# Kernel tuning notes

Measured on AMD Instinct MI355X. Metric: run time of the kernel, lower is better.

## Reference

```python
import jax, jax.numpy as jnp
import numpy as np

B, C2D, C3D, H, W, N = 4, 64, 64, 256, 256, 16384
NEG_SLOPE = 0.1


def _conv1x1_lrelu(x, w, b):
    # 1x1 conv (no norm) + leaky_relu(0.1), per Conv2dNormRelu defaults
    y = jnp.einsum('bchw,oc->bohw', x, w) + b[None, :, None, None]
    return jax.nn.leaky_relu(y, NEG_SLOPE)


def _batch_gather(feat, idx):
    # feat: [B, C, N], idx: [B, P] -> [B, C, P]
    return jnp.take_along_axis(feat, idx[:, None, :], axis=2)


def setup_inputs() -> dict:
    key = jax.random.key(0)
    ks = jax.random.split(key, 14)
    f = jax.random.normal
    s = 0.05
    return {
        'xy': jax.random.uniform(ks[0], (B, 2, N), jnp.float32) * jnp.float32(W),
        'feat_2d': f(ks[1], (B, C2D, H, W), jnp.float32),
        'feat_3d': f(ks[2], (B, C3D, N), jnp.float32),
        'last_flow_2d': f(ks[3], (B, 2, H, W), jnp.float32),
        'last_flow_3d_to_2d': f(ks[4], (B, 2, N), jnp.float32),
        'nn_proj': jax.random.randint(ks[5], (B, H, W, 1), 0, N, jnp.int32),
        'w1': f(ks[6], (C3D, C3D + 5), jnp.float32) * s,
        'b1': f(ks[7], (C3D,), jnp.float32) * s,
        'w2': f(ks[8], (C3D, C3D), jnp.float32) * s,
        'b2': f(ks[9], (C3D,), jnp.float32) * s,
        'w3': f(ks[10], (C3D, C3D), jnp.float32) * s,
        'b3': f(ks[11], (C3D,), jnp.float32) * s,
        'wf': f(ks[12], (C2D, C2D + C3D), jnp.float32) * s,
        'bf': f(ks[13], (C2D,), jnp.float32) * s,
    }


def reference(xy, feat_2d, feat_3d, last_flow_2d, last_flow_3d_to_2d, nn_proj,
              w1, b1, w2, b2, w3, b3, wf, bf):
    b, _, h, w = feat_2d.shape
    # concat per-point flow onto 3D features: [B, C3D+2, N]
    feat_3d_aug = jnp.concatenate([feat_3d, last_flow_3d_to_2d], axis=1)

    idx = nn_proj[..., 0].reshape(b, h * w)  # nearest-neighbor point per pixel
    gathered = _batch_gather(feat_3d_aug, idx).reshape(b, -1, h, w)  # [B, C3D+2, H, W]
    xy_proj = _batch_gather(xy, idx).reshape(b, 2, h, w)             # [B, 2, H, W]

    # pixel-coordinate mesh grid: channel 0 = x (width), channel 1 = y (height)
    gy, gx = jnp.meshgrid(jnp.arange(h, dtype=xy.dtype), jnp.arange(w, dtype=xy.dtype), indexing='ij')
    grid = jnp.stack([gx, gy], axis=0)[None]  # [1, 2, H, W]
    offset = xy_proj - grid                    # [B, 2, H, W]

    # correlation between gathered 3D feats and 2D feats (channel mean)
    corr = jnp.mean(gathered[:, :C2D] * feat_2d, axis=1, keepdims=True)  # [B, 1, H, W]

    # last 2 channels are the projected flow; subtract detached last_flow_2d
    flow_ch = gathered[:, -2:] - jax.lax.stop_gradient(last_flow_2d)
    x = jnp.concatenate([corr, offset, gathered[:, :-2], flow_ch], axis=1)  # [B, C3D+5, H, W]

    x = _conv1x1_lrelu(x, w1, b1)
    x = _conv1x1_lrelu(x, w2, b2)
    x = _conv1x1_lrelu(x, w3, b3)
    out = _conv1x1_lrelu(jnp.concatenate([x, feat_2d], axis=1), wf, bf)  # [B, C2D, H, W]
    return out
```

## Files before the change

### kernel.cpp

```cpp
#include <hip/hip_runtime.h>

#define BB 4
#define CH 64
#define HW 65536
#define NN 16384
#define NT 128
#define XPITCH 104
#define LPITCH 72
#define W1OFS 0
#define W2OFS 6144
#define W3OFS 10240
#define WFOFS 14336
#define FWS_BYTE 46080
#define PTAB_BYTE 49152
#define PT_ROW 160
#define WS_NEED ((size_t)PTAB_BYTE + (size_t)BB * NN * PT_ROW)

typedef __attribute__((ext_vector_type(8))) short short8;
typedef __attribute__((ext_vector_type(4))) float f32x4;

union frag_u { unsigned short u[8]; short8 v; };
union row_u  { uint4 q[4]; unsigned short u[32]; };
union half_u { uint4 q[2]; unsigned short u[16]; };

static __device__ __forceinline__ unsigned short f2bf(float x) {
    unsigned int u = __float_as_uint(x);
    return (unsigned short)((u + 0x7fffu + ((u >> 16) & 1u)) >> 16);
}
static __device__ __forceinline__ float bf2f(unsigned short h) {
    return __uint_as_float(((unsigned int)h) << 16);
}

__global__ __launch_bounds__(256) void prep_w(
    const float* __restrict__ w1, const float* __restrict__ b1,
    const float* __restrict__ w2, const float* __restrict__ b2,
    const float* __restrict__ w3, const float* __restrict__ b3,
    const float* __restrict__ wf, const float* __restrict__ bf,
    unsigned short* __restrict__ wpk, float* __restrict__ fws)
{
    const int t = threadIdx.x;
    const int blk = blockIdx.x;
    if (blk == 0) {
        for (int i = t; i < 64 * 96; i += 256) {
            const int m = i / 96, k = i % 96;
            float v = 0.f;
            if (k < 64) v = w1[m * 69 + 3 + k];
            else if (k == 64) v = w1[m * 69 + 0];
            else if (k == 67) v = w1[m * 69 + 67];
            else if (k == 68) v = w1[m * 69 + 68];
            wpk[W1OFS + i] = f2bf(v);
        }
    } else if (blk == 1) {
        for (int i = t; i < 64 * 64; i += 256) wpk[W2OFS + i] = f2bf(w2[i]);
    } else if (blk == 2) {
        for (int i = t; i < 64 * 64; i += 256) wpk[W3OFS + i] = f2bf(w3[i]);
    } else if (blk == 3) {
        for (int i = t; i < 64 * 128; i += 256) wpk[WFOFS + i] = f2bf(wf[i]);
    } else if (t < 64) {
        fws[t]       = b1[t];
        fws[64 + t]  = b2[t];
        fws[128 + t] = b3[t];
        fws[192 + t] = bf[t];
        fws[256 + t] = w1[t * 69 + 1];
        fws[320 + t] = w1[t * 69 + 2];
    }
}

__global__ __launch_bounds__(256) void prep_t(
    const float* __restrict__ xy, const float* __restrict__ f3d,
    const float* __restrict__ lf3d, char* __restrict__ pt)
{
    const int t = threadIdx.x;
    const int cq = t >> 6;
    const int l = t & 63;
    const int gn = blockIdx.x * 64 + l;
    const int b = blockIdx.y;
    half_u r;
#pragma unroll
    for (int i = 0; i < 16; i++)
        r.u[i] = f2bf(f3d[(size_t)(b * CH + cq * 16 + i) * NN + gn]);
    char* row = pt + ((size_t)b * NN + gn) * PT_ROW;
    uint4* rq = (uint4*)row;
    rq[2 * cq] = r.q[0];
    rq[2 * cq + 1] = r.q[1];
    if (cq == 0) {
        float4 e;
        e.x = xy[(size_t)(b * 2 + 0) * NN + gn];
        e.y = xy[(size_t)(b * 2 + 1) * NN + gn];
        e.z = lf3d[(size_t)(b * 2 + 0) * NN + gn];
        e.w = lf3d[(size_t)(b * 2 + 1) * NN + gn];
        *(float4*)(row + 144) = e;
    }
}

template<int KT, int KROW, bool LO>
static __device__ __forceinline__ void layer_mfma(
    const unsigned short* __restrict__ wrow,
    const unsigned short* Xh, const unsigned short* Xl,
    int w, int ln, int q, f32x4 acc[4][2])
{
#pragma unroll
    for (int kt = 0; kt < KT; kt++) {
        const int kcol = kt * 32 + q * 8;
        short8 A[4];
#pragma unroll
        for (int mi = 0; mi < 4; mi++)
            A[mi] = *(const short8*)(wrow + (mi * 16 + ln) * KROW + kcol);
#pragma unroll
        for (int ni = 0; ni < 2; ni++) {
            const int nr = 32 * w + ni * 16 + ln;
            short8 bh = *(const short8*)(Xh + nr * XPITCH + kcol);
            short8 bl = bh;
            if (LO) bl = *(const short8*)(Xl + nr * LPITCH + kcol);
#pragma unroll
            for (int mi = 0; mi < 4; mi++) {
                acc[mi][ni] = __builtin_amdgcn_mfma_f32_16x16x32_bf16(A[mi], bh, acc[mi][ni], 0, 0, 0);
                if (LO)
                    acc[mi][ni] = __builtin_amdgcn_mfma_f32_16x16x32_bf16(A[mi], bl, acc[mi][ni], 0, 0, 0);
            }
        }
    }
}

static __device__ __forceinline__ void zero_acc(f32x4 acc[4][2]) {
#pragma unroll
    for (int mi = 0; mi < 4; mi++)
#pragma unroll
        for (int ni = 0; ni < 2; ni++)
#pragma unroll
            for (int r = 0; r < 4; r++) acc[mi][ni][r] = 0.f;
}

static __device__ __forceinline__ void epi_x(
    f32x4 acc[4][2], const float* __restrict__ fws, int bofs, bool off_fix,
    const float* offsp, unsigned short* Xh, unsigned short* Xl,
    int w, int ln, int q)
{
#pragma unroll
    for (int mi = 0; mi < 4; mi++) {
        const float4 bias = *(const float4*)(fws + bofs + mi * 16 + q * 4);
        float4 wox = bias, woy = bias;
        if (off_fix) {
            wox = *(const float4*)(fws + 256 + mi * 16 + q * 4);
            woy = *(const float4*)(fws + 320 + mi * 16 + q * 4);
        }
#pragma unroll
        for (int ni = 0; ni < 2; ni++) {
            const int nr = 32 * w + ni * 16 + ln;
            float ox = 0.f, oy = 0.f;
            if (off_fix) { ox = offsp[nr]; oy = offsp[NT + nr]; }
            unsigned int hh0 = 0, hh1 = 0, ll0 = 0, ll1 = 0;
#pragma unroll
            for (int r = 0; r < 4; r++) {
                float a = acc[mi][ni][r] + ((const float*)&bias)[r];
                if (off_fix) a += ((const float*)&wox)[r] * ox + ((const float*)&woy)[r] * oy;
                a = fmaxf(a, 0.1f * a);
                const unsigned short hb = f2bf(a);
                const unsigned short lb = f2bf(a - bf2f(hb));
                if (r == 0) { hh0 = hb; ll0 = lb; }
                if (r == 1) { hh0 |= ((unsigned)hb) << 16; ll0 |= ((unsigned)lb) << 16; }
                if (r == 2) { hh1 = hb; ll1 = lb; }
                if (r == 3) { hh1 |= ((unsigned)hb) << 16; ll1 |= ((unsigned)lb) << 16; }
            }
            *(uint2*)&Xh[nr * XPITCH + mi * 16 + q * 4] = make_uint2(hh0, hh1);
            *(uint2*)&Xl[nr * LPITCH + mi * 16 + q * 4] = make_uint2(ll0, ll1);
        }
    }
}

__global__ __launch_bounds__(256, 3) void fuse(
    const float* __restrict__ feat2d, const float* __restrict__ lf2d,
    const int* __restrict__ nn,
    const unsigned short* __restrict__ wpk, const float* __restrict__ fws,
    const char* __restrict__ ptab,
    float* __restrict__ out)
{
    __shared__ unsigned short Xhi[NT * XPITCH];
    __shared__ unsigned short Xlo[NT * LPITCH];
    __shared__ float offsS[2 * NT];

    const int tid = threadIdx.x;
    const int w = tid >> 6, lane = tid & 63;
    const int q = lane >> 4, ln = lane & 15;
    const int b = blockIdx.y;
    const int p0 = blockIdx.x * NT;

    {
        const int cp = lane >> 5, j = lane & 31;
        const int n = 32 * w + j;
        const int p = p0 + n;
        const int idx = nn[(size_t)b * HW + p];
        const char* prow = ptab + ((size_t)b * NN + idx) * PT_ROW;
        row_u g;
#pragma unroll
        for (int k = 0; k < 4; k++) g.q[k] = ((const uint4*)prow)[cp * 4 + k];
        float ca = 0.f;
#pragma unroll
        for (int i = 0; i < 32; i++) {
            const int c = cp * 32 + i;
            ca += feat2d[(size_t)(b * CH + c) * HW + p] * bf2f(g.u[i]);
        }
        uint4* xp = (uint4*)&Xhi[n * XPITCH + cp * 32];
#pragma unroll
        for (int k = 0; k < 4; k++) xp[k] = g.q[k];
        ca += __shfl_xor(ca, 32);
        if (cp == 0) {
            const float4 e = *(const float4*)(prow + 144);
            offsS[n] = e.x - (float)(p & 255);
            offsS[NT + n] = e.y - (float)(p >> 8);
            const float fcx = e.z - lf2d[(size_t)(b * 2 + 0) * HW + p];
            const float fcy = e.w - lf2d[(size_t)(b * 2 + 1) * HW + p];
            const unsigned short chh = f2bf(ca * (1.0f / 64.0f));
            const unsigned short xhh = f2bf(fcx);
            const unsigned short yhh = f2bf(fcy);
            uint4* tp = (uint4*)&Xhi[n * XPITCH + 64];
            tp[0] = make_uint4((unsigned)chh, ((unsigned)xhh) << 16, (unsigned)yhh, 0u);
            tp[1] = make_uint4(0, 0, 0, 0);
            tp[2] = make_uint4(0, 0, 0, 0);
            tp[3] = make_uint4(0, 0, 0, 0);
        }
    }

    f32x4 acc[4][2];
    zero_acc(acc);
    layer_mfma<3, 96, false>(wpk + W1OFS, Xhi, Xlo, w, ln, q, acc);
    epi_x(acc, fws, 0, true, offsS, Xhi, Xlo, w, ln, q);
    zero_acc(acc);
    layer_mfma<2, 64, true>(wpk + W2OFS, Xhi, Xlo, w, ln, q, acc);
    epi_x(acc, fws, 64, false, offsS, Xhi, Xlo, w, ln, q);
    zero_acc(acc);
    layer_mfma<2, 64, true>(wpk + W3OFS, Xhi, Xlo, w, ln, q, acc);
    epi_x(acc, fws, 128, false, offsS, Xhi, Xlo, w, ln, q);
    zero_acc(acc);
    layer_mfma<2, 128, true>(wpk + WFOFS, Xhi, Xlo, w, ln, q, acc);
#pragma unroll
    for (int kt = 2; kt < 4; kt++) {
        const int kcol = kt * 32 + q * 8;
        short8 A[4];
#pragma unroll
        for (int mi = 0; mi < 4; mi++)
            A[mi] = *(const short8*)(wpk + WFOFS + (mi * 16 + ln) * 128 + kcol);
#pragma unroll
        for (int ni = 0; ni < 2; ni++) {
            frag_u fh;
#pragma unroll
            for (int j = 0; j < 8; j++) {
                const int c = (kt - 2) * 32 + q * 8 + j;
                const float v = feat2d[(size_t)(b * CH + c) * HW + p0 + 32 * w + ni * 16 + ln];
                fh.u[j] = f2bf(v);
            }
#pragma unroll
            for (int mi = 0; mi < 4; mi++)
                acc[mi][ni] = __builtin_amdgcn_mfma_f32_16x16x32_bf16(A[mi], fh.v, acc[mi][ni], 0, 0, 0);
        }
    }
#pragma unroll
    for (int mi = 0; mi < 4; mi++) {
        const float4 bias = *(const float4*)(fws + 192 + mi * 16 + q * 4);
#pragma unroll
        for (int ni = 0; ni < 2; ni++) {
#pragma unroll
            for (int r = 0; r < 4; r++) {
                float a = acc[mi][ni][r] + ((const float*)&bias)[r];
                a = fmaxf(a, 0.1f * a);
                const int m = mi * 16 + q * 4 + r;
                out[(size_t)(b * CH + m) * HW + p0 + 32 * w + ni * 16 + ln] = a;
            }
        }
    }
}

__global__ __launch_bounds__(256) void fuse_slow(
    const float* __restrict__ feat2d, const float* __restrict__ lf2d,
    const float* __restrict__ xy, const float* __restrict__ feat3d,
    const float* __restrict__ lf3d, const int* __restrict__ nn,
    const float* __restrict__ w1, const float* __restrict__ b1,
    const float* __restrict__ w2, const float* __restrict__ b2,
    const float* __restrict__ w3, const float* __restrict__ b3,
    const float* __restrict__ wf, const float* __restrict__ bfv,
    float* __restrict__ out)
{
    const int p = blockIdx.x * 256 + threadIdx.x;
    const int b = blockIdx.y;
    const int idx = nn[(size_t)b * HW + p];
    const float* f3 = feat3d + (size_t)b * CH * NN + idx;
    float g[CH];
#pragma unroll
    for (int c = 0; c < CH; c++) g[c] = f3[(size_t)c * NN];
    const float fl3x = lf3d[(size_t)(b * 2 + 0) * NN + idx];
    const float fl3y = lf3d[(size_t)(b * 2 + 1) * NN + idx];
    const float xyx = xy[(size_t)(b * 2 + 0) * NN + idx];
    const float xyy = xy[(size_t)(b * 2 + 1) * NN + idx];
    const float* f2p = feat2d + (size_t)b * CH * HW + p;
    float corr = 0.f;
#pragma unroll
    for (int c = 0; c < CH; c++) corr += f2p[(size_t)c * HW] * g[c];
    corr *= (1.f / 64.f);
    float xin[69];
    xin[0] = corr;
    xin[1] = xyx - (float)(p & 255);
    xin[2] = xyy - (float)(p >> 8);
#pragma unroll
    for (int c = 0; c < CH; c++) xin[3 + c] = g[c];
    xin[67] = fl3x - lf2d[(size_t)(b * 2 + 0) * HW + p];
    xin[68] = fl3y - lf2d[(size_t)(b * 2 + 1) * HW + p];
    float x1[64], x2[64], x3[64], accv[64];
#pragma unroll
    for (int o = 0; o < 64; o++) {
        float a = b1[o];
#pragma unroll
        for (int k = 0; k < 69; k++) a += w1[o * 69 + k] * xin[k];
        x1[o] = (a >= 0.f) ? a : 0.1f * a;
    }
#pragma unroll
    for (int o = 0; o < 64; o++) {
        float a = b2[o];
#pragma unroll
        for (int k = 0; k < 64; k++) a += w2[o * 64 + k] * x1[k];
        x2[o] = (a >= 0.f) ? a : 0.1f * a;
    }
#pragma unroll
    for (int o = 0; o < 64; o++) {
        float a = b3[o];
#pragma unroll
        for (int k = 0; k < 64; k++) a += w3[o * 64 + k] * x2[k];
        x3[o] = (a >= 0.f) ? a : 0.1f * a;
    }
#pragma unroll
    for (int o = 0; o < 64; o++) {
        float a = bfv[o];
#pragma unroll
        for (int k = 0; k < 64; k++) a += wf[o * 128 + k] * x3[k];
        accv[o] = a;
    }
#pragma unroll
    for (int k = 0; k < 64; k++) {
        const float f = f2p[(size_t)k * HW];
#pragma unroll
        for (int o = 0; o < 64; o++) accv[o] += wf[o * 128 + 64 + k] * f;
    }
#pragma unroll
    for (int o = 0; o < 64; o++) {
        float a = accv[o];
        a = (a >= 0.f) ? a : 0.1f * a;
        out[(size_t)(b * CH + o) * HW + p] = a;
    }
}

extern "C" void kernel_launch(void* const* d_in, const int* in_sizes, int n_in,
                              void* d_out, int out_size, void* d_ws, size_t ws_size,
                              hipStream_t stream)
{
    const float* xy   = (const float*)d_in[0];
    const float* f2d  = (const float*)d_in[1];
    const float* f3d  = (const float*)d_in[2];
    const float* lf2d = (const float*)d_in[3];
    const float* lf3d = (const float*)d_in[4];
    const int*   nn   = (const int*)d_in[5];
    const float* w1 = (const float*)d_in[6];
    const float* b1 = (const float*)d_in[7];
    const float* w2 = (const float*)d_in[8];
    const float* b2 = (const float*)d_in[9];
    const float* w3 = (const float*)d_in[10];
    const float* b3 = (const float*)d_in[11];
    const float* wf = (const float*)d_in[12];
    const float* bf = (const float*)d_in[13];

    if (ws_size >= WS_NEED) {
        unsigned short* wpk = (unsigned short*)d_ws;
        float* fws = (float*)((char*)d_ws + FWS_BYTE);
        char* pt = (char*)d_ws + PTAB_BYTE;
        prep_w<<<dim3(5), 256, 0, stream>>>(w1, b1, w2, b2, w3, b3, wf, bf, wpk, fws);
        prep_t<<<dim3(NN / 64, BB), 256, 0, stream>>>(xy, f3d, lf3d, pt);
        fuse<<<dim3(HW / NT, BB), 256, 0, stream>>>(f2d, lf2d, nn, wpk, fws, pt, (float*)d_out);
    } else {
        fuse_slow<<<dim3(HW / 256, BB), 256, 0, stream>>>(f2d, lf2d, xy, f3d, lf3d, nn,
                                                          w1, b1, w2, b2, w3, b3, wf, bf,
                                                          (float*)d_out);
    }
}
```

Baseline: 237.4 us.

## Fold corr and flow channels of layer 1 into fp32 epilogue, shrink K

Moves the three extra layer-1 inputs (correlation, two flow-difference channels) out of the padded 96-wide bf16 K dimension and applies them as rank-1 fp32 updates in the epilogue, like the offset channels already were. Layer 1 now runs a 64-wide MFMA K loop, the Xhi pitch drops from 104 to 72, and the packed weight offsets shift to match. The smaller shared footprint lets the launch bound ask for 4 blocks per SM instead of 3. The cost is a few extra FMAs and shared loads in the first epilogue and tighter register limits, which could cause spills.

```diff
diff --git a/kernel.cpp b/kernel.cpp
--- a/kernel.cpp
+++ b/kernel.cpp
@@ -5,12 +5,12 @@
 #define HW 65536
 #define NN 16384
 #define NT 128
-#define XPITCH 104
+#define XPITCH 72
 #define LPITCH 72
 #define W1OFS 0
-#define W2OFS 6144
-#define W3OFS 10240
-#define WFOFS 14336
+#define W2OFS 4096
+#define W3OFS 8192
+#define WFOFS 12288
 #define FWS_BYTE 46080
 #define PTAB_BYTE 49152
 #define PT_ROW 160
@@ -41,14 +41,9 @@
     const int t = threadIdx.x;
     const int blk = blockIdx.x;
     if (blk == 0) {
-        for (int i = t; i < 64 * 96; i += 256) {
-            const int m = i / 96, k = i % 96;
-            float v = 0.f;
-            if (k < 64) v = w1[m * 69 + 3 + k];
-            else if (k == 64) v = w1[m * 69 + 0];
-            else if (k == 67) v = w1[m * 69 + 67];
-            else if (k == 68) v = w1[m * 69 + 68];
-            wpk[W1OFS + i] = f2bf(v);
+        for (int i = t; i < 64 * 64; i += 256) {
+            const int m = i >> 6, k = i & 63;
+            wpk[W1OFS + i] = f2bf(w1[m * 69 + 3 + k]);
         }
     } else if (blk == 1) {
         for (int i = t; i < 64 * 64; i += 256) wpk[W2OFS + i] = f2bf(w2[i]);
@@ -63,6 +58,9 @@
         fws[192 + t] = bf[t];
         fws[256 + t] = w1[t * 69 + 1];
         fws[320 + t] = w1[t * 69 + 2];
+        fws[384 + t] = w1[t * 69 + 0];
+        fws[448 + t] = w1[t * 69 + 67];
+        fws[512 + t] = w1[t * 69 + 68];
     }
 }
 
@@ -133,27 +131,37 @@
 
 static __device__ __forceinline__ void epi_x(
     f32x4 acc[4][2], const float* __restrict__ fws, int bofs, bool off_fix,
-    const float* offsp, unsigned short* Xh, unsigned short* Xl,
+    const float* offsp, const float* auxp, unsigned short* Xh, unsigned short* Xl,
     int w, int ln, int q)
 {
 #pragma unroll
     for (int mi = 0; mi < 4; mi++) {
         const float4 bias = *(const float4*)(fws + bofs + mi * 16 + q * 4);
-        float4 wox = bias, woy = bias;
+        float4 wox = bias, woy = bias, wco = bias, wfx = bias, wfy = bias;
         if (off_fix) {
             wox = *(const float4*)(fws + 256 + mi * 16 + q * 4);
             woy = *(const float4*)(fws + 320 + mi * 16 + q * 4);
+            wco = *(const float4*)(fws + 384 + mi * 16 + q * 4);
+            wfx = *(const float4*)(fws + 448 + mi * 16 + q * 4);
+            wfy = *(const float4*)(fws + 512 + mi * 16 + q * 4);
         }
 #pragma unroll
         for (int ni = 0; ni < 2; ni++) {
             const int nr = 32 * w + ni * 16 + ln;
-            float ox = 0.f, oy = 0.f;
-            if (off_fix) { ox = offsp[nr]; oy = offsp[NT + nr]; }
+            float ox = 0.f, oy = 0.f, co = 0.f, fx = 0.f, fy = 0.f;
+            if (off_fix) {
+                ox = offsp[nr]; oy = offsp[NT + nr];
+                co = auxp[nr];  fx = auxp[NT + nr]; fy = auxp[2 * NT + nr];
+            }
             unsigned int hh0 = 0, hh1 = 0, ll0 = 0, ll1 = 0;
 #pragma unroll
             for (int r = 0; r < 4; r++) {
                 float a = acc[mi][ni][r] + ((const float*)&bias)[r];
-                if (off_fix) a += ((const float*)&wox)[r] * ox + ((const float*)&woy)[r] * oy;
+                if (off_fix) {
+                    a += ((const float*)&wox)[r] * ox + ((const float*)&woy)[r] * oy;
+                    a += ((const float*)&wco)[r] * co;
+                    a += ((const float*)&wfx)[r] * fx + ((const float*)&wfy)[r] * fy;
+                }
                 a = fmaxf(a, 0.1f * a);
                 const unsigned short hb = f2bf(a);
                 const unsigned short lb = f2bf(a - bf2f(hb));
@@ -168,7 +176,7 @@
     }
 }
 
-__global__ __launch_bounds__(256, 3) void fuse(
+__global__ __launch_bounds__(256, 4) void fuse(
     const float* __restrict__ feat2d, const float* __restrict__ lf2d,
     const int* __restrict__ nn,
     const unsigned short* __restrict__ wpk, const float* __restrict__ fws,
@@ -178,6 +186,7 @@
     __shared__ unsigned short Xhi[NT * XPITCH];
     __shared__ unsigned short Xlo[NT * LPITCH];
     __shared__ float offsS[2 * NT];
+    __shared__ float auxS[3 * NT];
 
     const int tid = threadIdx.x;
     const int w = tid >> 6, lane = tid & 63;
@@ -208,29 +217,22 @@
             const float4 e = *(const float4*)(prow + 144);
             offsS[n] = e.x - (float)(p & 255);
             offsS[NT + n] = e.y - (float)(p >> 8);
-            const float fcx = e.z - lf2d[(size_t)(b * 2 + 0) * HW + p];
-            const float fcy = e.w - lf2d[(size_t)(b * 2 + 1) * HW + p];
-            const unsigned short chh = f2bf(ca * (1.0f / 64.0f));
-            const unsigned short xhh = f2bf(fcx);
-            const unsigned short yhh = f2bf(fcy);
-            uint4* tp = (uint4*)&Xhi[n * XPITCH + 64];
-            tp[0] = make_uint4((unsigned)chh, ((unsigned)xhh) << 16, (unsigned)yhh, 0u);
-            tp[1] = make_uint4(0, 0, 0, 0);
-            tp[2] = make_uint4(0, 0, 0, 0);
-            tp[3] = make_uint4(0, 0, 0, 0);
+            auxS[n] = ca * (1.0f / 64.0f);
+            auxS[NT + n] = e.z - lf2d[(size_t)(b * 2 + 0) * HW + p];
+            auxS[2 * NT + n] = e.w - lf2d[(size_t)(b * 2 + 1) * HW + p];
         }
     }
 
     f32x4 acc[4][2];
     zero_acc(acc);
-    layer_mfma<3, 96, false>(wpk + W1OFS, Xhi, Xlo, w, ln, q, acc);
-    epi_x(acc, fws, 0, true, offsS, Xhi, Xlo, w, ln, q);
+    layer_mfma<2, 64, false>(wpk + W1OFS, Xhi, Xlo, w, ln, q, acc);
+    epi_x(acc, fws, 0, true, offsS, auxS, Xhi, Xlo, w, ln, q);
     zero_acc(acc);
     layer_mfma<2, 64, true>(wpk + W2OFS, Xhi, Xlo, w, ln, q, acc);
-    epi_x(acc, fws, 64, false, offsS, Xhi, Xlo, w, ln, q);
+    epi_x(acc, fws, 64, false, offsS, auxS, Xhi, Xlo, w, ln, q);
     zero_acc(acc);
     layer_mfma<2, 64, true>(wpk + W3OFS, Xhi, Xlo, w, ln, q, acc);
-    epi_x(acc, fws, 128, false, offsS, Xhi, Xlo, w, ln, q);
+    epi_x(acc, fws, 128, false, offsS, auxS, Xhi, Xlo, w, ln, q);
     zero_acc(acc);
     layer_mfma<2, 128, true>(wpk + WFOFS, Xhi, Xlo, w, ln, q, acc);
 #pragma unroll
```

After: 227.1 us. -4.3%, faster.
